# Kernel tuning notes

Measured on AMD Instinct MI355X. Metric: run time of the kernel, lower is better.

## Reference

```python
import jax, jax.numpy as jnp
import numpy as np
import math

F = 64        # num_features (multiplicity of each irrep)
N = 16000     # nodes
E = 256000    # edges (avg_num_neighbors = 16)
S = 4         # num_species
DE = 32       # scalar edge feature dim (radial basis)
W = 128       # interaction_mlp_width
AVG_NEIGH = 16.0
SQ2 = math.sqrt(2.0)
SQ3 = math.sqrt(3.0)


def setup_inputs() -> dict:
    key = jax.random.key(0)
    ks = jax.random.split(key, 32)
    def nrm(k, shape, scale=1.0):
        return jax.random.normal(k, shape, dtype=jnp.float32) * scale
    inp = {}
    # forward args
    inp["vectors"] = nrm(ks[0], (E, 1, 3))
    inp["lengths"] = jax.random.uniform(ks[1], (E, 1), dtype=jnp.float32)
    inp["node_s"] = nrm(ks[2], (N, F))            # 64x0e part of node_feats
    inp["node_v"] = nrm(ks[3], (N, F, 3))         # 64x1o part of node_feats
    inp["scalar_edge_feats"] = nrm(ks[4], (E, DE))
    inp["node_specie"] = jax.random.randint(ks[5], (N,), 0, S)
    inp["senders"] = jax.random.randint(ks[6], (E,), 0, N)
    inp["receivers"] = jax.random.randint(ks[7], (E,), 0, N)
    # parameters (e3nn Linear = per-irrep channel mixing, fan-in normalized; bias only on 0e)
    inp["W_up_s"] = nrm(ks[8], (F, F), F ** -0.5); inp["b_up_s"] = jnp.zeros((F,), jnp.float32)
    inp["W_up_v"] = nrm(ks[9], (F, F), F ** -0.5)
    din = 2 * F + DE + 1
    inp["mlp_W1"] = nrm(ks[10], (din, W), din ** -0.5); inp["mlp_b1"] = jnp.zeros((W,), jnp.float32)
    inp["mlp_W2"] = nrm(ks[11], (W, W), W ** -0.5); inp["mlp_b2"] = jnp.zeros((W,), jnp.float32)
    inp["mlp_W3"] = nrm(ks[12], (W, 3 * F), W ** -0.5); inp["mlp_b3"] = jnp.zeros((3 * F,), jnp.float32)
    inp["W_dn_s"] = nrm(ks[13], (F, F), F ** -0.5); inp["b_dn_s"] = jnp.zeros((F,), jnp.float32)
    inp["W_dn_v"] = nrm(ks[14], (2 * F, F), (2 * F) ** -0.5)
    # symmetric contraction weights (per species, per channel); correlation=2
    inp["w_sc_s"] = nrm(ks[15], (S, 3, F), 3 ** -0.5)   # paths to 0e: x0, x0^2, (x1.x1)/sqrt3
    inp["w_sc_v"] = nrm(ks[16], (S, 2, F), 2 ** -0.5)   # paths to 1o: x1, x0*x1
    inp["W_pb_s"] = nrm(ks[17], (F, F), F ** -0.5); inp["b_pb_s"] = jnp.zeros((F,), jnp.float32)
    inp["W_pb_v"] = nrm(ks[18], (F, F), F ** -0.5)
    inp["W_r1_s"] = nrm(ks[19], (F, 2 * F), F ** -0.5); inp["b_r1_s"] = jnp.zeros((2 * F,), jnp.float32)
    inp["W_r1_v"] = nrm(ks[20], (F, F), F ** -0.5)
    inp["W_r2_s"] = nrm(ks[21], (F, 1), F ** -0.5); inp["b_r2"] = jnp.zeros((1,), jnp.float32)
    inp["W_r2_v"] = nrm(ks[22], (F, 1), F ** -0.5)
    return inp


def reference(vectors, lengths, node_s, node_v, scalar_edge_feats, node_specie,
              senders, receivers,
              W_up_s, b_up_s, W_up_v,
              mlp_W1, mlp_b1, mlp_W2, mlp_b2, mlp_W3, mlp_b3,
              W_dn_s, b_dn_s, W_dn_v,
              w_sc_s, w_sc_v, W_pb_s, b_pb_s, W_pb_v,
              W_r1_s, b_r1_s, W_r1_v, W_r2_s, b_r2, W_r2_v):
    n = node_s.shape[0]
    # --- spherical harmonics, sh_irreps='1o', component normalization, normalize=False ---
    edge_v = SQ3 * vectors[:, 0, :]                              # [E,3]

    # --- InteractionBlock: linear_up ---
    h_s = node_s @ W_up_s + b_up_s                               # [N,F]
    h_v = jnp.einsum('nfi,fg->ngi', node_v, W_up_v)              # [N,F,3]

    # --- MessagePassingConvolution ---
    m_s = h_s[senders]                                           # [E,F] 0e
    m_v = h_v[senders]                                           # [E,F,3] 1o
    # tensor product with edge 1o, filtered to 0e+1o (unitary CG):
    tp_s = jnp.einsum('efi,ei->ef', m_v, edge_v) / SQ3           # 1o x 1o -> 0e  [E,F]
    tp_v1 = m_s[:, :, None] * edge_v[:, None, :]                 # 0e x 1o -> 1o  [E,F,3]
    tp_v2 = jnp.cross(m_v, edge_v[:, None, :]) / SQ2             # 1o x 1o -> 1o  [E,F,3]
    # scalar MLP mix (one scalar weight per output irrep = 3F)
    mlp_in = jnp.concatenate([m_s, h_s[receivers], scalar_edge_feats, lengths], axis=1)
    h = jax.nn.silu(mlp_in @ mlp_W1 + mlp_b1)
    h = jax.nn.silu(h @ mlp_W2 + mlp_b2)
    mix = h @ mlp_W3 + mlp_b3                                    # [E,3F]
    mix_s, mix_v1, mix_v2 = mix[:, :F], mix[:, F:2 * F], mix[:, 2 * F:]
    tp_s = tp_s * mix_s
    tp_v = jnp.concatenate([tp_v1 * mix_v1[:, :, None], tp_v2 * mix_v2[:, :, None]], axis=1)  # [E,2F,3]
    # scatter-add to receivers, normalize by avg_num_neighbors
    agg_s = jax.ops.segment_sum(tp_s, receivers, num_segments=n) / AVG_NEIGH   # [N,F]
    agg_v = jax.ops.segment_sum(tp_v, receivers, num_segments=n) / AVG_NEIGH   # [N,2F,3]
    # linear_down
    f_s = agg_s @ W_dn_s + b_dn_s                                # [N,F]
    f_v = jnp.einsum('nfi,fg->ngi', agg_v, W_dn_v)               # [N,F,3]

    # --- EquivariantProductBasisBlock: symmetric contraction (correlation=2), per-species ---
    ws = w_sc_s[node_specie]                                     # [N,3,F]
    wv = w_sc_v[node_specie]                                     # [N,2,F]
    vv = jnp.sum(f_v * f_v, axis=-1) / SQ3                       # 1o (x) 1o -> 0e, symmetric
    sc_s = ws[:, 0] * f_s + ws[:, 1] * (f_s * f_s) + ws[:, 2] * vv           # [N,F]
    sc_v = wv[:, 0][:, :, None] * f_v + wv[:, 1][:, :, None] * (f_s[:, :, None] * f_v)  # [N,F,3]
    p_s = sc_s @ W_pb_s + b_pb_s                                 # node_feats 0e out
    p_v = jnp.einsum('nfi,fg->ngi', sc_v, W_pb_v)                # node_feats 1o out

    # --- NonLinearReadoutBlock: linear to (2F x 0e + F x 1o), gate, linear to 1x0e+1x1o ---
    r_s = p_s @ W_r1_s + b_r1_s                                  # [N,2F]
    r_v = jnp.einsum('nfi,fg->ngi', p_v, W_r1_v)                 # [N,F,3]
    act = jax.nn.silu(r_s[:, :F])
    gates = jax.nn.silu(r_s[:, F:])
    g_v = gates[:, :, None] * r_v                                # gated vectors
    out_s = act @ W_r2_s + b_r2                                  # [N,1]  0e output
    out_v = jnp.einsum('nfi,fo->noi', g_v, W_r2_v)               # [N,1,3] 1o output
    return out_s, out_v, p_s, p_v
```

## Files before the change

kernel.cpp:

```cpp
#include <hip/hip_runtime.h>

typedef short bf16x8 __attribute__((ext_vector_type(8)));
typedef float f32x4  __attribute__((ext_vector_type(4)));
typedef unsigned short ushort_t;

__device__ __forceinline__ float silu(float x) {
    float t = __expf(-x);
    return x * __builtin_amdgcn_rcpf(1.f + t);
}

__device__ __forceinline__ ushort_t f2bs(float x) {
    union { float f; unsigned int u; } v; v.f = x;
    unsigned int r = v.u + 0x7FFF + ((v.u >> 16) & 1);
    return (ushort_t)(r >> 16);
}
__device__ __forceinline__ ushort_t f2bs_t(float x) {
    union { float f; unsigned int u; } v; v.f = x;
    return (ushort_t)(v.u >> 16);
}
__device__ __forceinline__ float bs2f(ushort_t x) {
    union { unsigned int u; float f; } v; v.u = ((unsigned int)x) << 16; return v.f;
}

constexpr int N_   = 16000;
constexpr int E_   = 256000;
constexpr int Fd   = 64;

constexpr float SQ3f    = 1.7320508075688772f;
constexpr float INV_SQ3 = 0.5773502691896258f;
constexpr float INV_SQ2 = 0.7071067811865476f;
constexpr float INV_AVG = 0.0625f;

constexpr int OFF_OS = 0;
constexpr int OFF_OV = N_;
constexpr int OFF_PS = OFF_OV + 3 * N_;
constexpr int OFF_PV = OFF_PS + N_ * Fd;

constexpr int W1P_SZ = 6 * 8 * 512;
constexpr int W2P_SZ = 4 * 8 * 512;
constexpr int W3P_SZ = 4 * 12 * 512;

__global__ __launch_bounds__(256) void pack_kernel(
    const float* __restrict__ W1, const float* __restrict__ W2,
    const float* __restrict__ W3,
    ushort_t* __restrict__ W1p, ushort_t* __restrict__ W2p,
    ushort_t* __restrict__ W3p)
{
    int idx = blockIdx.x * 256 + threadIdx.x;
    if (idx < W1P_SZ) {
        int j = idx & 7, lane = (idx >> 3) & 63, tile = idx >> 9;
        int c = tile >> 3, t = tile & 7;
        int k = c * 32 + (lane >> 4) * 8 + j;
        int n = t * 16 + (lane & 15);
        W1p[idx] = f2bs(k < 161 ? W1[k * 128 + n] : 0.f);
    } else if (idx < W1P_SZ + W2P_SZ) {
        int q = idx - W1P_SZ;
        int j = q & 7, lane = (q >> 3) & 63, tile = q >> 9;
        int c = tile >> 3, t = tile & 7;
        int k = c * 32 + (lane >> 4) * 8 + j;
        int n = t * 16 + (lane & 15);
        W2p[q] = f2bs(W2[k * 128 + n]);
    } else {
        int q = idx - W1P_SZ - W2P_SZ;
        int j = q & 7, lane = (q >> 3) & 63, tile = q >> 9;
        int c = tile / 12, t = tile % 12;
        int k = c * 32 + (lane >> 4) * 8 + j;
        int n = t * 16 + (lane & 15);
        W3p[q] = f2bs(W3[k * 192 + n]);
    }
}

__global__ __launch_bounds__(64) void up_kernel(
    const float* __restrict__ node_s, const float* __restrict__ node_v,
    const float* __restrict__ W_up_s, const float* __restrict__ b_up_s,
    const float* __restrict__ W_up_v,
    const int* __restrict__ receivers, int* __restrict__ cnt,
    ushort_t* __restrict__ hs_bf, float* __restrict__ h_v)
{
    __shared__ float ns[Fd];
    __shared__ float nv[Fd][3];
    const int n = blockIdx.x;
    const int g = threadIdx.x;

    if (g < 16) {
        int e = n * 16 + g;
        atomicAdd(&cnt[receivers[e]], 1);
    }

    ns[g] = node_s[n * Fd + g];
    for (int idx = g; idx < Fd * 3; idx += 64)
        nv[idx / 3][idx % 3] = node_v[n * Fd * 3 + idx];
    __syncthreads();

    float as = b_up_s[g];
    float a0 = 0.f, a1 = 0.f, a2 = 0.f;
    #pragma unroll 8
    for (int f = 0; f < Fd; f++) {
        float wss = W_up_s[f * Fd + g];
        as += ns[f] * wss;
        float wv = W_up_v[f * Fd + g];
        a0 += nv[f][0] * wv;
        a1 += nv[f][1] * wv;
        a2 += nv[f][2] * wv;
    }
    hs_bf[n * Fd + g] = f2bs(as);
    h_v[n * 192 + 0 * 64 + g] = a0;
    h_v[n * 192 + 1 * 64 + g] = a1;
    h_v[n * 192 + 2 * 64 + g] = a2;
}

__global__ __launch_bounds__(1024) void scan_kernel(
    const int* __restrict__ cnt, int* __restrict__ base, int* __restrict__ cursor)
{
    __shared__ int part[1024];
    const int t = threadIdx.x;
    int v[16];
    int s = 0;
    if (t < 1000) {
        const int4* c4 = (const int4*)(cnt + t * 16);
        #pragma unroll
        for (int q = 0; q < 4; q++) {
            int4 w = c4[q];
            v[q * 4 + 0] = w.x; v[q * 4 + 1] = w.y;
            v[q * 4 + 2] = w.z; v[q * 4 + 3] = w.w;
            s += w.x + w.y + w.z + w.w;
        }
    }
    part[t] = s;
    __syncthreads();
    for (int off = 1; off < 1024; off <<= 1) {
        int u = (t >= off) ? part[t - off] : 0;
        __syncthreads();
        part[t] += u;
        __syncthreads();
    }
    if (t < 1000) {
        int run = part[t] - s;
        int b[16];
        #pragma unroll
        for (int i = 0; i < 16; i++) { b[i] = run; run += v[i]; }
        int4* bb = (int4*)(base + t * 16);
        int4* cc = (int4*)(cursor + t * 16);
        #pragma unroll
        for (int q = 0; q < 4; q++) {
            int4 w = { b[q * 4], b[q * 4 + 1], b[q * 4 + 2], b[q * 4 + 3] };
            bb[q] = w;
            cc[q] = w;
        }
    }
}

__global__ __launch_bounds__(256, 6) void edge_mlp_kernel(
    const float* __restrict__ lengths, const float* __restrict__ sef,
    const int* __restrict__ senders, const int* __restrict__ receivers,
    const float* __restrict__ b1f, const float* __restrict__ b2f,
    const float* __restrict__ b3f,
    const ushort_t* __restrict__ hs_bf,
    const ushort_t* __restrict__ W1p, const ushort_t* __restrict__ W2p,
    const ushort_t* __restrict__ W3p,
    int* __restrict__ cursor, int* __restrict__ sorted_eid,
    ushort_t* __restrict__ tpx)
{
    __shared__ ushort_t Hs[64 * 136];

    const int tid  = threadIdx.x;
    const int wave = tid >> 6, lane = tid & 63;
    const int quad = lane >> 4, l4 = lane & 15;
    const int ebase = blockIdx.x * 64 + wave * 16;
    const int me    = ebase + l4;
    const int hrow  = wave * 16;

    if (tid < 64) {
        int e = blockIdx.x * 64 + tid;
        int p = atomicAdd(&cursor[receivers[e]], 1);
        sorted_eid[p] = e;
    }

    const int snd = senders[me];
    const int rcv = receivers[me];

    bf16x8 a[6];
    a[0] = *(const bf16x8*)(hs_bf + snd * 64 + quad * 8);
    a[1] = *(const bf16x8*)(hs_bf + snd * 64 + 32 + quad * 8);
    a[2] = *(const bf16x8*)(hs_bf + rcv * 64 + quad * 8);
    a[3] = *(const bf16x8*)(hs_bf + rcv * 64 + 32 + quad * 8);
    {
        const float4 s0 = *(const float4*)(sef + (size_t)me * 32 + quad * 8);
        const float4 s1 = *(const float4*)(sef + (size_t)me * 32 + quad * 8 + 4);
        bf16x8 t;
        t[0] = (short)f2bs(s0.x); t[1] = (short)f2bs(s0.y);
        t[2] = (short)f2bs(s0.z); t[3] = (short)f2bs(s0.w);
        t[4] = (short)f2bs(s1.x); t[5] = (short)f2bs(s1.y);
        t[6] = (short)f2bs(s1.z); t[7] = (short)f2bs(s1.w);
        a[4] = t;
    }
    {
        bf16x8 t = {0, 0, 0, 0, 0, 0, 0, 0};
        if (quad == 0) t[0] = (short)f2bs(lengths[me]);
        a[5] = t;
    }

    const bf16x8* B1 = (const bf16x8*)W1p;
    const bf16x8* B2 = (const bf16x8*)W2p;
    const bf16x8* B3 = (const bf16x8*)W3p;

    f32x4 acc[8];
    #pragma unroll
    for (int t = 0; t < 8; t++) acc[t] = (f32x4){0.f, 0.f, 0.f, 0.f};
    #pragma unroll
    for (int c = 0; c < 6; c++) {
        #pragma unroll
        for (int t = 0; t < 8; t++)
            acc[t] = __builtin_amdgcn_mfma_f32_16x16x32_bf16(
                a[c], B1[(c * 8 + t) * 64 + lane], acc[t], 0, 0, 0);
    }
    #pragma unroll
    for (int t = 0; t < 8; t++) {
        float bb = b1f[t * 16 + l4];
        #pragma unroll
        for (int r = 0; r < 4; r++)
            Hs[(hrow + quad * 4 + r) * 136 + t * 16 + l4] = f2bs_t(silu(acc[t][r] + bb));
    }

    #pragma unroll
    for (int t = 0; t < 8; t++) acc[t] = (f32x4){0.f, 0.f, 0.f, 0.f};
    #pragma unroll
    for (int c = 0; c < 4; c++) {
        bf16x8 af = *(const bf16x8*)(&Hs[(hrow + l4) * 136 + c * 32 + quad * 8]);
        #pragma unroll
        for (int t = 0; t < 8; t++)
            acc[t] = __builtin_amdgcn_mfma_f32_16x16x32_bf16(
                af, B2[(c * 8 + t) * 64 + lane], acc[t], 0, 0, 0);
    }
    #pragma unroll
    for (int t = 0; t < 8; t++) {
        float bb = b2f[t * 16 + l4];
        #pragma unroll
        for (int r = 0; r < 4; r++)
            Hs[(hrow + quad * 4 + r) * 136 + t * 16 + l4] = f2bs_t(silu(acc[t][r] + bb));
    }

    f32x4 acc3[12];
    #pragma unroll
    for (int t = 0; t < 12; t++) acc3[t] = (f32x4){0.f, 0.f, 0.f, 0.f};
    #pragma unroll
    for (int c = 0; c < 4; c++) {
        bf16x8 af = *(const bf16x8*)(&Hs[(hrow + l4) * 136 + c * 32 + quad * 8]);
        #pragma unroll
        for (int t = 0; t < 12; t++)
            acc3[t] = __builtin_amdgcn_mfma_f32_16x16x32_bf16(
                af, B3[(c * 12 + t) * 64 + lane], acc3[t], 0, 0, 0);
    }
    #pragma unroll
    for (int t = 0; t < 12; t++) {
        float bb = b3f[t * 16 + l4];
        #pragma unroll
        for (int r = 0; r < 4; r++)
            tpx[(size_t)(ebase + quad * 4 + r) * 192 + t * 16 + l4] =
                f2bs(acc3[t][r] + bb);
    }
}

__global__ __launch_bounds__(64, 8) void node_fused_kernel(
    const int* __restrict__ base, const int* __restrict__ cnt,
    const int* __restrict__ sorted_eid, const int* __restrict__ senders,
    const float* __restrict__ vectors,
    const ushort_t* __restrict__ tpx,
    const ushort_t* __restrict__ hs_bf, const float* __restrict__ h_v,
    const int* __restrict__ specie,
    const float* __restrict__ W_dn_s, const float* __restrict__ b_dn_s,
    const float* __restrict__ W_dn_v,
    const float* __restrict__ w_sc_s, const float* __restrict__ w_sc_v,
    const float* __restrict__ W_pb_s, const float* __restrict__ b_pb_s,
    const float* __restrict__ W_pb_v,
    const float* __restrict__ W_r1_s, const float* __restrict__ b_r1_s,
    const float* __restrict__ W_r1_v,
    const float* __restrict__ W_r2_s, const float* __restrict__ b_r2,
    const float* __restrict__ W_r2_v,
    float* __restrict__ out)
{
    __shared__ float as_l[Fd];
    __shared__ float av_l[2 * Fd][3];
    __shared__ float scs[Fd];
    __shared__ float scv[Fd][3];
    __shared__ float ps[Fd];
    __shared__ float pv[Fd][3];
    __shared__ int   eids[64];

    const int n = blockIdx.x;
    const int g = threadIdx.x;

    const int b = base[n];
    const int c = cnt[n];
    float accS = 0.f;
    float a10 = 0.f, a11 = 0.f, a12 = 0.f;
    float a20 = 0.f, a21 = 0.f, a22 = 0.f;

    for (int done = 0; done < c; done += 64) {
        int m = min(64, c - done);
        __syncthreads();
        if (g < m) eids[g] = sorted_eid[b + done + g];
        __syncthreads();
        for (int i = 0; i < m; i++) {
            const int e  = eids[i];
            const int se = senders[e];
            const float ev0 = SQ3f * vectors[e * 3 + 0];
            const float ev1 = SQ3f * vectors[e * 3 + 1];
            const float ev2 = SQ3f * vectors[e * 3 + 2];
            const float mv0 = h_v[(size_t)se * 192 + 0 * 64 + g];
            const float mv1 = h_v[(size_t)se * 192 + 1 * 64 + g];
            const float mv2 = h_v[(size_t)se * 192 + 2 * 64 + g];
            const float m_s = bs2f(hs_bf[se * 64 + g]);
            const ushort_t* mrow = tpx + (size_t)e * 192;
            const float c0 = bs2f(mrow[g]);
            const float c1 = bs2f(mrow[64 + g]);
            const float c2 = bs2f(mrow[128 + g]);

            float dot = mv0 * ev0 + mv1 * ev1 + mv2 * ev2;
            accS += dot * c0;
            float k1 = m_s * c1;
            a10 += k1 * ev0; a11 += k1 * ev1; a12 += k1 * ev2;
            a20 += (mv1 * ev2 - mv2 * ev1) * c2;
            a21 += (mv2 * ev0 - mv0 * ev2) * c2;
            a22 += (mv0 * ev1 - mv1 * ev0) * c2;
        }
    }
    as_l[g] = accS * (INV_SQ3 * INV_AVG);
    av_l[g][0] = a10 * INV_AVG;
    av_l[g][1] = a11 * INV_AVG;
    av_l[g][2] = a12 * INV_AVG;
    av_l[64 + g][0] = a20 * (INV_SQ2 * INV_AVG);
    av_l[64 + g][1] = a21 * (INV_SQ2 * INV_AVG);
    av_l[64 + g][2] = a22 * (INV_SQ2 * INV_AVG);
    __syncthreads();

    float f_s = b_dn_s[g];
    #pragma unroll 8
    for (int f = 0; f < Fd; f++) f_s += as_l[f] * W_dn_s[f * Fd + g];
    float fv0 = 0.f, fv1 = 0.f, fv2 = 0.f;
    #pragma unroll 8
    for (int f = 0; f < 2 * Fd; f++) {
        float w = W_dn_v[f * Fd + g];
        fv0 += av_l[f][0] * w;
        fv1 += av_l[f][1] * w;
        fv2 += av_l[f][2] * w;
    }

    float vv = (fv0 * fv0 + fv1 * fv1 + fv2 * fv2) * INV_SQ3;
    int sp = specie[n];
    float ws0 = w_sc_s[sp * 3 * Fd + 0 * Fd + g];
    float ws1 = w_sc_s[sp * 3 * Fd + 1 * Fd + g];
    float ws2 = w_sc_s[sp * 3 * Fd + 2 * Fd + g];
    float wv0 = w_sc_v[sp * 2 * Fd + 0 * Fd + g];
    float wv1 = w_sc_v[sp * 2 * Fd + 1 * Fd + g];
    float sc_s = ws0 * f_s + ws1 * f_s * f_s + ws2 * vv;
    float kv = wv0 + wv1 * f_s;
    scs[g] = sc_s;
    scv[g][0] = kv * fv0;
    scv[g][1] = kv * fv1;
    scv[g][2] = kv * fv2;
    __syncthreads();

    float p_s = b_pb_s[g];
    float pv0 = 0.f, pv1 = 0.f, pv2 = 0.f;
    #pragma unroll 8
    for (int f = 0; f < Fd; f++) {
        float wps = W_pb_s[f * Fd + g];
        p_s += scs[f] * wps;
        float wpv = W_pb_v[f * Fd + g];
        pv0 += scv[f][0] * wpv;
        pv1 += scv[f][1] * wpv;
        pv2 += scv[f][2] * wpv;
    }
    ps[g] = p_s;
    pv[g][0] = pv0; pv[g][1] = pv1; pv[g][2] = pv2;

    out[OFF_PS + n * Fd + g] = p_s;
    out[OFF_PV + (size_t)n * Fd * 3 + g * 3 + 0] = pv0;
    out[OFF_PV + (size_t)n * Fd * 3 + g * 3 + 1] = pv1;
    out[OFF_PV + (size_t)n * Fd * 3 + g * 3 + 2] = pv2;
    __syncthreads();

    float r0 = b_r1_s[g];
    float r1 = b_r1_s[g + Fd];
    float rv0 = 0.f, rv1 = 0.f, rv2 = 0.f;
    #pragma unroll 8
    for (int f = 0; f < Fd; f++) {
        float p = ps[f];
        r0 += p * W_r1_s[f * 2 * Fd + g];
        r1 += p * W_r1_s[f * 2 * Fd + g + Fd];
        float wrv = W_r1_v[f * Fd + g];
        rv0 += pv[f][0] * wrv;
        rv1 += pv[f][1] * wrv;
        rv2 += pv[f][2] * wrv;
    }
    float act  = silu(r0);
    float gate = silu(r1);
    float o_s = act * W_r2_s[g];
    float wr2v = W_r2_v[g];
    float ov0 = gate * rv0 * wr2v;
    float ov1 = gate * rv1 * wr2v;
    float ov2 = gate * rv2 * wr2v;

    #pragma unroll
    for (int off = 32; off > 0; off >>= 1) {
        o_s += __shfl_down(o_s, off);
        ov0 += __shfl_down(ov0, off);
        ov1 += __shfl_down(ov1, off);
        ov2 += __shfl_down(ov2, off);
    }
    if (g == 0) {
        out[OFF_OS + n] = o_s + b_r2[0];
        out[OFF_OV + n * 3 + 0] = ov0;
        out[OFF_OV + n * 3 + 1] = ov1;
        out[OFF_OV + n * 3 + 2] = ov2;
    }
}

extern "C" void kernel_launch(void* const* d_in, const int* in_sizes, int n_in,
                              void* d_out, int out_size, void* d_ws, size_t ws_size,
                              hipStream_t stream)
{
    const float* vectors  = (const float*)d_in[0];
    const float* lengths  = (const float*)d_in[1];
    const float* node_s   = (const float*)d_in[2];
    const float* node_v   = (const float*)d_in[3];
    const float* sef      = (const float*)d_in[4];
    const int*  specie    = (const int*)d_in[5];
    const int*  senders   = (const int*)d_in[6];
    const int*  receivers = (const int*)d_in[7];
    const float* W_up_s   = (const float*)d_in[8];
    const float* b_up_s   = (const float*)d_in[9];
    const float* W_up_v   = (const float*)d_in[10];
    const float* mlp_W1   = (const float*)d_in[11];
    const float* mlp_b1   = (const float*)d_in[12];
    const float* mlp_W2   = (const float*)d_in[13];
    const float* mlp_b2   = (const float*)d_in[14];
    const float* mlp_W3   = (const float*)d_in[15];
    const float* mlp_b3   = (const float*)d_in[16];
    const float* W_dn_s   = (const float*)d_in[17];
    const float* b_dn_s   = (const float*)d_in[18];
    const float* W_dn_v   = (const float*)d_in[19];
    const float* w_sc_s   = (const float*)d_in[20];
    const float* w_sc_v   = (const float*)d_in[21];
    const float* W_pb_s   = (const float*)d_in[22];
    const float* b_pb_s   = (const float*)d_in[23];
    const float* W_pb_v   = (const float*)d_in[24];
    const float* W_r1_s   = (const float*)d_in[25];
    const float* b_r1_s   = (const float*)d_in[26];
    const float* W_r1_v   = (const float*)d_in[27];
    const float* W_r2_s   = (const float*)d_in[28];
    const float* b_r2     = (const float*)d_in[29];
    const float* W_r2_v   = (const float*)d_in[30];

    float* h_v = (float*)d_ws;
    ushort_t* tpx   = (ushort_t*)(h_v + (size_t)N_ * 192);
    ushort_t* hs_bf = tpx + (size_t)E_ * 192;
    ushort_t* W1p   = hs_bf + (size_t)N_ * 64;
    ushort_t* W2p   = W1p + W1P_SZ;
    ushort_t* W3p   = W2p + W2P_SZ;
    int* cnt        = (int*)((((size_t)(W3p + W3P_SZ)) + 15) & ~(size_t)15);
    int* base       = cnt + N_;
    int* cursor     = base + N_;
    int* sorted_eid = cursor + N_;

    float* out = (float*)d_out;

    hipMemsetAsync(cnt, 0, N_ * sizeof(int), stream);

    up_kernel<<<N_, 64, 0, stream>>>(node_s, node_v, W_up_s, b_up_s, W_up_v,
                                     receivers, cnt, hs_bf, h_v);
    pack_kernel<<<256, 256, 0, stream>>>(mlp_W1, mlp_W2, mlp_W3, W1p, W2p, W3p);
    scan_kernel<<<1, 1024, 0, stream>>>(cnt, base, cursor);

    edge_mlp_kernel<<<E_ / 64, 256, 0, stream>>>(
        lengths, sef, senders, receivers,
        mlp_b1, mlp_b2, mlp_b3,
        hs_bf, W1p, W2p, W3p, cursor, sorted_eid, tpx);

    node_fused_kernel<<<N_, 64, 0, stream>>>(
        base, cnt, sorted_eid, senders, vectors,
        tpx, hs_bf, h_v, specie,
        W_dn_s, b_dn_s, W_dn_v, w_sc_s, w_sc_v,
        W_pb_s, b_pb_s, W_pb_v, W_r1_s, b_r1_s, W_r1_v,
        W_r2_s, b_r2, W_r2_v, out);
}
```

Measured before the change: 413.6 us.

## Process multiple nodes/edges per wave to reuse weight loads across rows

The up and node kernels now handle four nodes per 64-thread block, so each weight element loaded from global memory is reused across four nodes. The edge MLP gives each wave 32 edges (two 16-row MFMA tiles) sharing each B fragment, with 128-thread blocks. This cuts repeated weight traffic and block count in exchange for more registers, lower occupancy, and serialized per-node edge loops in the node kernel.

```diff
diff --git a/kernel.cpp b/kernel.cpp
--- a/kernel.cpp
+++ b/kernel.cpp
@@ -70,43 +70,54 @@
     }
 }
 
-__global__ __launch_bounds__(64) void up_kernel(
+__global__ __launch_bounds__(64, 4) void up_kernel(
     const float* __restrict__ node_s, const float* __restrict__ node_v,
     const float* __restrict__ W_up_s, const float* __restrict__ b_up_s,
     const float* __restrict__ W_up_v,
     const int* __restrict__ receivers, int* __restrict__ cnt,
     ushort_t* __restrict__ hs_bf, float* __restrict__ h_v)
 {
-    __shared__ float ns[Fd];
-    __shared__ float nv[Fd][3];
-    const int n = blockIdx.x;
-    const int g = threadIdx.x;
-
-    if (g < 16) {
-        int e = n * 16 + g;
+    __shared__ float ns[4][64];
+    __shared__ float nv[4][64][3];
+    const int n0 = blockIdx.x * 4;
+    const int g  = threadIdx.x;
+
+    {
+        int e = blockIdx.x * 64 + g;
         atomicAdd(&cnt[receivers[e]], 1);
     }
 
-    ns[g] = node_s[n * Fd + g];
-    for (int idx = g; idx < Fd * 3; idx += 64)
-        nv[idx / 3][idx % 3] = node_v[n * Fd * 3 + idx];
+    #pragma unroll
+    for (int j = 0; j < 4; j++) ns[j][g] = node_s[(n0 + j) * 64 + g];
+    for (int idx = g; idx < 4 * 192; idx += 64) {
+        int j = idx / 192, r = idx - j * 192;
+        nv[j][r / 3][r % 3] = node_v[(size_t)n0 * 192 + idx];
+    }
     __syncthreads();
 
-    float as = b_up_s[g];
-    float a0 = 0.f, a1 = 0.f, a2 = 0.f;
-    #pragma unroll 8
-    for (int f = 0; f < Fd; f++) {
-        float wss = W_up_s[f * Fd + g];
-        as += ns[f] * wss;
-        float wv = W_up_v[f * Fd + g];
-        a0 += nv[f][0] * wv;
-        a1 += nv[f][1] * wv;
-        a2 += nv[f][2] * wv;
-    }
-    hs_bf[n * Fd + g] = f2bs(as);
-    h_v[n * 192 + 0 * 64 + g] = a0;
-    h_v[n * 192 + 1 * 64 + g] = a1;
-    h_v[n * 192 + 2 * 64 + g] = a2;
+    float as[4], a0[4], a1[4], a2[4];
+    float bb = b_up_s[g];
+    #pragma unroll
+    for (int j = 0; j < 4; j++) { as[j] = bb; a0[j] = a1[j] = a2[j] = 0.f; }
+    #pragma unroll 4
+    for (int f = 0; f < 64; f++) {
+        float wss = W_up_s[f * 64 + g];
+        float wv  = W_up_v[f * 64 + g];
+        #pragma unroll
+        for (int j = 0; j < 4; j++) {
+            as[j] += ns[j][f] * wss;
+            a0[j] += nv[j][f][0] * wv;
+            a1[j] += nv[j][f][1] * wv;
+            a2[j] += nv[j][f][2] * wv;
+        }
+    }
+    #pragma unroll
+    for (int j = 0; j < 4; j++) {
+        hs_bf[(n0 + j) * 64 + g] = f2bs(as[j]);
+        h_v[(n0 + j) * 192 + 0 * 64 + g] = a0[j];
+        h_v[(n0 + j) * 192 + 1 * 64 + g] = a1[j];
+        h_v[(n0 + j) * 192 + 2 * 64 + g] = a2[j];
+    }
 }
 
 __global__ __launch_bounds__(1024) void scan_kernel(
@@ -150,7 +161,7 @@
     }
 }
 
-__global__ __launch_bounds__(256, 6) void edge_mlp_kernel(
+__global__ __launch_bounds__(128, 2) void edge_mlp_kernel(
     const float* __restrict__ lengths, const float* __restrict__ sef,
     const int* __restrict__ senders, const int* __restrict__ receivers,
     const float* __restrict__ b1f, const float* __restrict__ b2f,
@@ -166,9 +177,10 @@
     const int tid  = threadIdx.x;
     const int wave = tid >> 6, lane = tid & 63;
     const int quad = lane >> 4, l4 = lane & 15;
-    const int ebase = blockIdx.x * 64 + wave * 16;
-    const int me    = ebase + l4;
-    const int hrow  = wave * 16;
+    const int ebase = blockIdx.x * 64 + wave * 32;
+    const int me0   = ebase + l4;
+    const int me1   = ebase + 16 + l4;
+    const int hrow  = wave * 32;
 
     if (tid < 64) {
         int e = blockIdx.x * 64 + tid;
@@ -176,92 +188,117 @@
         sorted_eid[p] = e;
     }
 
-    const int snd = senders[me];
-    const int rcv = receivers[me];
-
-    bf16x8 a[6];
-    a[0] = *(const bf16x8*)(hs_bf + snd * 64 + quad * 8);
-    a[1] = *(const bf16x8*)(hs_bf + snd * 64 + 32 + quad * 8);
-    a[2] = *(const bf16x8*)(hs_bf + rcv * 64 + quad * 8);
-    a[3] = *(const bf16x8*)(hs_bf + rcv * 64 + 32 + quad * 8);
+    const int snd0 = senders[me0], rcv0 = receivers[me0];
+    const int snd1 = senders[me1], rcv1 = receivers[me1];
+
+    bf16x8 a0[6], a1[6];
+    a0[0] = *(const bf16x8*)(hs_bf + snd0 * 64 + quad * 8);
+    a0[1] = *(const bf16x8*)(hs_bf + snd0 * 64 + 32 + quad * 8);
+    a0[2] = *(const bf16x8*)(hs_bf + rcv0 * 64 + quad * 8);
+    a0[3] = *(const bf16x8*)(hs_bf + rcv0 * 64 + 32 + quad * 8);
+    a1[0] = *(const bf16x8*)(hs_bf + snd1 * 64 + quad * 8);
+    a1[1] = *(const bf16x8*)(hs_bf + snd1 * 64 + 32 + quad * 8);
+    a1[2] = *(const bf16x8*)(hs_bf + rcv1 * 64 + quad * 8);
+    a1[3] = *(const bf16x8*)(hs_bf + rcv1 * 64 + 32 + quad * 8);
     {
-        const float4 s0 = *(const float4*)(sef + (size_t)me * 32 + quad * 8);
-        const float4 s1 = *(const float4*)(sef + (size_t)me * 32 + quad * 8 + 4);
+        const float4 s0 = *(const float4*)(sef + (size_t)me0 * 32 + quad * 8);
+        const float4 s1 = *(const float4*)(sef + (size_t)me0 * 32 + quad * 8 + 4);
         bf16x8 t;
         t[0] = (short)f2bs(s0.x); t[1] = (short)f2bs(s0.y);
         t[2] = (short)f2bs(s0.z); t[3] = (short)f2bs(s0.w);
         t[4] = (short)f2bs(s1.x); t[5] = (short)f2bs(s1.y);
         t[6] = (short)f2bs(s1.z); t[7] = (short)f2bs(s1.w);
-        a[4] = t;
+        a0[4] = t;
+        const float4 u0 = *(const float4*)(sef + (size_t)me1 * 32 + quad * 8);
+        const float4 u1 = *(const float4*)(sef + (size_t)me1 * 32 + quad * 8 + 4);
+        t[0] = (short)f2bs(u0.x); t[1] = (short)f2bs(u0.y);
+        t[2] = (short)f2bs(u0.z); t[3] = (short)f2bs(u0.w);
+        t[4] = (short)f2bs(u1.x); t[5] = (short)f2bs(u1.y);
+        t[6] = (short)f2bs(u1.z); t[7] = (short)f2bs(u1.w);
+        a1[4] = t;
     }
     {
-        bf16x8 t = {0, 0, 0, 0, 0, 0, 0, 0};
-        if (quad == 0) t[0] = (short)f2bs(lengths[me]);
-        a[5] = t;
+        bf16x8 t = {0,0,0,0,0,0,0,0};
+        bf16x8 u = {0,0,0,0,0,0,0,0};
+        if (quad == 0) { t[0] = (short)f2bs(lengths[me0]); u[0] = (short)f2bs(lengths[me1]); }
+        a0[5] = t; a1[5] = u;
     }
 
     const bf16x8* B1 = (const bf16x8*)W1p;
     const bf16x8* B2 = (const bf16x8*)W2p;
     const bf16x8* B3 = (const bf16x8*)W3p;
 
-    f32x4 acc[8];
-    #pragma unroll
-    for (int t = 0; t < 8; t++) acc[t] = (f32x4){0.f, 0.f, 0.f, 0.f};
+    f32x4 accA[8], accB[8];
+    #pragma unroll
+    for (int t = 0; t < 8; t++) { accA[t] = (f32x4){0,0,0,0}; accB[t] = (f32x4){0,0,0,0}; }
     #pragma unroll
     for (int c = 0; c < 6; c++) {
         #pragma unroll
-        for (int t = 0; t < 8; t++)
-            acc[t] = __builtin_amdgcn_mfma_f32_16x16x32_bf16(
-                a[c], B1[(c * 8 + t) * 64 + lane], acc[t], 0, 0, 0);
+        for (int t = 0; t < 8; t++) {
+            bf16x8 b = B1[(c * 8 + t) * 64 + lane];
+            accA[t] = __builtin_amdgcn_mfma_f32_16x16x32_bf16(a0[c], b, accA[t], 0, 0, 0);
+            accB[t] = __builtin_amdgcn_mfma_f32_16x16x32_bf16(a1[c], b, accB[t], 0, 0, 0);
+        }
     }
     #pragma unroll
     for (int t = 0; t < 8; t++) {
         float bb = b1f[t * 16 + l4];
         #pragma unroll
-        for (int r = 0; r < 4; r++)
-            Hs[(hrow + quad * 4 + r) * 136 + t * 16 + l4] = f2bs_t(silu(acc[t][r] + bb));
-    }
-
-    #pragma unroll
-    for (int t = 0; t < 8; t++) acc[t] = (f32x4){0.f, 0.f, 0.f, 0.f};
+        for (int r = 0; r < 4; r++) {
+            Hs[(hrow + quad * 4 + r) * 136 + t * 16 + l4]      = f2bs_t(silu(accA[t][r] + bb));
+            Hs[(hrow + 16 + quad * 4 + r) * 136 + t * 16 + l4] = f2bs_t(silu(accB[t][r] + bb));
+        }
+    }
+
+    #pragma unroll
+    for (int t = 0; t < 8; t++) { accA[t] = (f32x4){0,0,0,0}; accB[t] = (f32x4){0,0,0,0}; }
     #pragma unroll
     for (int c = 0; c < 4; c++) {
-        bf16x8 af = *(const bf16x8*)(&Hs[(hrow + l4) * 136 + c * 32 + quad * 8]);
-        #pragma unroll
-        for (int t = 0; t < 8; t++)
-            acc[t] = __builtin_amdgcn_mfma_f32_16x16x32_bf16(
-                af, B2[(c * 8 + t) * 64 + lane], acc[t], 0, 0, 0);
+        bf16x8 af0 = *(const bf16x8*)(&Hs[(hrow + l4) * 136 + c * 32 + quad * 8]);
+        bf16x8 af1 = *(const bf16x8*)(&Hs[(hrow + 16 + l4) * 136 + c * 32 + quad * 8]);
+        #pragma unroll
+        for (int t = 0; t < 8; t++) {
+            bf16x8 b = B2[(c * 8 + t) * 64 + lane];
+            accA[t] = __builtin_amdgcn_mfma_f32_16x16x32_bf16(af0, b, accA[t], 0, 0, 0);
+            accB[t] = __builtin_amdgcn_mfma_f32_16x16x32_bf16(af1, b, accB[t], 0, 0, 0);
+        }
     }
     #pragma unroll
     for (int t = 0; t < 8; t++) {
         float bb = b2f[t * 16 + l4];
         #pragma unroll
-        for (int r = 0; r < 4; r++)
-            Hs[(hrow + quad * 4 + r) * 136 + t * 16 + l4] = f2bs_t(silu(acc[t][r] + bb));
-    }
-
-    f32x4 acc3[12];
-    #pragma unroll
-    for (int t = 0; t < 12; t++) acc3[t] = (f32x4){0.f, 0.f, 0.f, 0.f};
+        for (int r = 0; r < 4; r++) {
+            Hs[(hrow + quad * 4 + r) * 136 + t * 16 + l4]      = f2bs_t(silu(accA[t][r] + bb));
+            Hs[(hrow + 16 + quad * 4 + r) * 136 + t * 16 + l4] = f2bs_t(silu(accB[t][r] + bb));
+        }
+    }
+
+    f32x4 acc3A[12], acc3B[12];
+    #pragma unroll
+    for (int t = 0; t < 12; t++) { acc3A[t] = (f32x4){0,0,0,0}; acc3B[t] = (f32x4){0,0,0,0}; }
     #pragma unroll
     for (int c = 0; c < 4; c++) {
-        bf16x8 af = *(const bf16x8*)(&Hs[(hrow + l4) * 136 + c * 32 + quad * 8]);
-        #pragma unroll
-        for (int t = 0; t < 12; t++)
-            acc3[t] = __builtin_amdgcn_mfma_f32_16x16x32_bf16(
-                af, B3[(c * 12 + t) * 64 + lane], acc3[t], 0, 0, 0);
+        bf16x8 af0 = *(const bf16x8*)(&Hs[(hrow + l4) * 136 + c * 32 + quad * 8]);
+        bf16x8 af1 = *(const bf16x8*)(&Hs[(hrow + 16 + l4) * 136 + c * 32 + quad * 8]);
+        #pragma unroll
+        for (int t = 0; t < 12; t++) {
+            bf16x8 b = B3[(c * 12 + t) * 64 + lane];
+            acc3A[t] = __builtin_amdgcn_mfma_f32_16x16x32_bf16(af0, b, acc3A[t], 0, 0, 0);
+            acc3B[t] = __builtin_amdgcn_mfma_f32_16x16x32_bf16(af1, b, acc3B[t], 0, 0, 0);
+        }
     }
     #pragma unroll
     for (int t = 0; t < 12; t++) {
         float bb = b3f[t * 16 + l4];
         #pragma unroll
-        for (int r = 0; r < 4; r++)
-            tpx[(size_t)(ebase + quad * 4 + r) * 192 + t * 16 + l4] =
-                f2bs(acc3[t][r] + bb);
-    }
-}
-
-__global__ __launch_bounds__(64, 8) void node_fused_kernel(
+        for (int r = 0; r < 4; r++) {
+            tpx[(size_t)(ebase + quad * 4 + r) * 192 + t * 16 + l4]      = f2bs(acc3A[t][r] + bb);
+            tpx[(size_t)(ebase + 16 + quad * 4 + r) * 192 + t * 16 + l4] = f2bs(acc3B[t][r] + bb);
+        }
+    }
+}
+
+__global__ __launch_bounds__(64, 4) void node_fused_kernel(
     const int* __restrict__ base, const int* __restrict__ cnt,
     const int* __restrict__ sorted_eid, const int* __restrict__ senders,
     const float* __restrict__ vectors,
@@ -279,141 +316,177 @@
     const float* __restrict__ W_r2_v,
     float* __restrict__ out)
 {
-    __shared__ float as_l[Fd];
-    __shared__ float av_l[2 * Fd][3];
-    __shared__ float scs[Fd];
-    __shared__ float scv[Fd][3];
-    __shared__ float ps[Fd];
-    __shared__ float pv[Fd][3];
+    __shared__ float as_l[4][64];
+    __shared__ float av_l[4][128][3];
+    __shared__ float scs[4][64];
+    __shared__ float scv[4][64][3];
+    __shared__ float ps_[4][64];
+    __shared__ float pv_[4][64][3];
     __shared__ int   eids[64];
 
-    const int n = blockIdx.x;
-    const int g = threadIdx.x;
-
-    const int b = base[n];
-    const int c = cnt[n];
-    float accS = 0.f;
-    float a10 = 0.f, a11 = 0.f, a12 = 0.f;
-    float a20 = 0.f, a21 = 0.f, a22 = 0.f;
-
-    for (int done = 0; done < c; done += 64) {
-        int m = min(64, c - done);
-        __syncthreads();
-        if (g < m) eids[g] = sorted_eid[b + done + g];
-        __syncthreads();
-        for (int i = 0; i < m; i++) {
-            const int e  = eids[i];
-            const int se = senders[e];
-            const float ev0 = SQ3f * vectors[e * 3 + 0];
-            const float ev1 = SQ3f * vectors[e * 3 + 1];
-            const float ev2 = SQ3f * vectors[e * 3 + 2];
-            const float mv0 = h_v[(size_t)se * 192 + 0 * 64 + g];
-            const float mv1 = h_v[(size_t)se * 192 + 1 * 64 + g];
-            const float mv2 = h_v[(size_t)se * 192 + 2 * 64 + g];
-            const float m_s = bs2f(hs_bf[se * 64 + g]);
-            const ushort_t* mrow = tpx + (size_t)e * 192;
-            const float c0 = bs2f(mrow[g]);
-            const float c1 = bs2f(mrow[64 + g]);
-            const float c2 = bs2f(mrow[128 + g]);
-
-            float dot = mv0 * ev0 + mv1 * ev1 + mv2 * ev2;
-            accS += dot * c0;
-            float k1 = m_s * c1;
-            a10 += k1 * ev0; a11 += k1 * ev1; a12 += k1 * ev2;
-            a20 += (mv1 * ev2 - mv2 * ev1) * c2;
-            a21 += (mv2 * ev0 - mv0 * ev2) * c2;
-            a22 += (mv0 * ev1 - mv1 * ev0) * c2;
-        }
-    }
-    as_l[g] = accS * (INV_SQ3 * INV_AVG);
-    av_l[g][0] = a10 * INV_AVG;
-    av_l[g][1] = a11 * INV_AVG;
-    av_l[g][2] = a12 * INV_AVG;
-    av_l[64 + g][0] = a20 * (INV_SQ2 * INV_AVG);
-    av_l[64 + g][1] = a21 * (INV_SQ2 * INV_AVG);
-    av_l[64 + g][2] = a22 * (INV_SQ2 * INV_AVG);
+    const int n0 = blockIdx.x * 4;
+    const int g  = threadIdx.x;
+
+    for (int j = 0; j < 4; j++) {
+        const int n = n0 + j;
+        const int b = base[n];
+        const int c = cnt[n];
+        float accS = 0.f;
+        float a10 = 0.f, a11 = 0.f, a12 = 0.f;
+        float a20 = 0.f, a21 = 0.f, a22 = 0.f;
+
+        for (int done = 0; done < c; done += 64) {
+            int m = min(64, c - done);
+            __syncthreads();
+            if (g < m) eids[g] = sorted_eid[b + done + g];
+            __syncthreads();
+            for (int i = 0; i < m; i++) {
+                const int e  = eids[i];
+                const int se = senders[e];
+                const float ev0 = SQ3f * vectors[e * 3 + 0];
+                const float ev1 = SQ3f * vectors[e * 3 + 1];
+                const float ev2 = SQ3f * vectors[e * 3 + 2];
+                const float mv0 = h_v[(size_t)se * 192 + 0 * 64 + g];
+                const float mv1 = h_v[(size_t)se * 192 + 1 * 64 + g];
+                const float mv2 = h_v[(size_t)se * 192 + 2 * 64 + g];
+                const float m_s = bs2f(hs_bf[se * 64 + g]);
+                const ushort_t* mrow = tpx + (size_t)e * 192;
+                const float c0 = bs2f(mrow[g]);
+                const float c1 = bs2f(mrow[64 + g]);
+                const float c2 = bs2f(mrow[128 + g]);
+
+                float dot = mv0 * ev0 + mv1 * ev1 + mv2 * ev2;
+                accS += dot * c0;
+                float k1 = m_s * c1;
+                a10 += k1 * ev0; a11 += k1 * ev1; a12 += k1 * ev2;
+                a20 += (mv1 * ev2 - mv2 * ev1) * c2;
+                a21 += (mv2 * ev0 - mv0 * ev2) * c2;
+                a22 += (mv0 * ev1 - mv1 * ev0) * c2;
+            }
+        }
+        as_l[j][g] = accS * (INV_SQ3 * INV_AVG);
+        av_l[j][g][0] = a10 * INV_AVG;
+        av_l[j][g][1] = a11 * INV_AVG;
+        av_l[j][g][2] = a12 * INV_AVG;
+        av_l[j][64 + g][0] = a20 * (INV_SQ2 * INV_AVG);
+        av_l[j][64 + g][1] = a21 * (INV_SQ2 * INV_AVG);
+        av_l[j][64 + g][2] = a22 * (INV_SQ2 * INV_AVG);
+    }
     __syncthreads();
 
-    float f_s = b_dn_s[g];
-    #pragma unroll 8
-    for (int f = 0; f < Fd; f++) f_s += as_l[f] * W_dn_s[f * Fd + g];
-    float fv0 = 0.f, fv1 = 0.f, fv2 = 0.f;
-    #pragma unroll 8
-    for (int f = 0; f < 2 * Fd; f++) {
-        float w = W_dn_v[f * Fd + g];
-        fv0 += av_l[f][0] * w;
-        fv1 += av_l[f][1] * w;
-        fv2 += av_l[f][2] * w;
-    }
-
-    float vv = (fv0 * fv0 + fv1 * fv1 + fv2 * fv2) * INV_SQ3;
-    int sp = specie[n];
-    float ws0 = w_sc_s[sp * 3 * Fd + 0 * Fd + g];
-    float ws1 = w_sc_s[sp * 3 * Fd + 1 * Fd + g];
-    float ws2 = w_sc_s[sp * 3 * Fd + 2 * Fd + g];
-    float wv0 = w_sc_v[sp * 2 * Fd + 0 * Fd + g];
-    float wv1 = w_sc_v[sp * 2 * Fd + 1 * Fd + g];
-    float sc_s = ws0 * f_s + ws1 * f_s * f_s + ws2 * vv;
-    float kv = wv0 + wv1 * f_s;
-    scs[g] = sc_s;
-    scv[g][0] = kv * fv0;
-    scv[g][1] = kv * fv1;
-    scv[g][2] = kv * fv2;
+    float f_s[4];
+    {
+        float bb = b_dn_s[g];
+        #pragma unroll
+        for (int j = 0; j < 4; j++) f_s[j] = bb;
+    }
+    #pragma unroll 4
+    for (int f = 0; f < 64; f++) {
+        float w = W_dn_s[f * 64 + g];
+        #pragma unroll
+        for (int j = 0; j < 4; j++) f_s[j] += as_l[j][f] * w;
+    }
+    float fv[4][3] = {};
+    #pragma unroll 4
+    for (int f = 0; f < 128; f++) {
+        float w = W_dn_v[f * 64 + g];
+        #pragma unroll
+        for (int j = 0; j < 4; j++) {
+            fv[j][0] += av_l[j][f][0] * w;
+            fv[j][1] += av_l[j][f][1] * w;
+            fv[j][2] += av_l[j][f][2] * w;
+        }
+    }
+
+    #pragma unroll
+    for (int j = 0; j < 4; j++) {
+        float vv = (fv[j][0]*fv[j][0] + fv[j][1]*fv[j][1] + fv[j][2]*fv[j][2]) * INV_SQ3;
+        int sp = specie[n0 + j];
+        float ws0 = w_sc_s[sp * 192 + 0 * 64 + g];
+        float ws1 = w_sc_s[sp * 192 + 1 * 64 + g];
+        float ws2 = w_sc_s[sp * 192 + 2 * 64 + g];
+        float wv0 = w_sc_v[sp * 128 + 0 * 64 + g];
+        float wv1 = w_sc_v[sp * 128 + 1 * 64 + g];
+        float sc = ws0 * f_s[j] + ws1 * f_s[j] * f_s[j] + ws2 * vv;
+        float kv = wv0 + wv1 * f_s[j];
+        scs[j][g] = sc;
+        scv[j][g][0] = kv * fv[j][0];
+        scv[j][g][1] = kv * fv[j][1];
+        scv[j][g][2] = kv * fv[j][2];
+    }
     __syncthreads();
 
-    float p_s = b_pb_s[g];
-    float pv0 = 0.f, pv1 = 0.f, pv2 = 0.f;
-    #pragma unroll 8
-    for (int f = 0; f < Fd; f++) {
-        float wps = W_pb_s[f * Fd + g];
-        p_s += scs[f] * wps;
-        float wpv = W_pb_v[f * Fd + g];
-        pv0 += scv[f][0] * wpv;
-        pv1 += scv[f][1] * wpv;
-        pv2 += scv[f][2] * wpv;
-    }
-    ps[g] = p_s;
-    pv[g][0] = pv0; pv[g][1] = pv1; pv[g][2] = pv2;
-
-    out[OFF_PS + n * Fd + g] = p_s;
-    out[OFF_PV + (size_t)n * Fd * 3 + g * 3 + 0] = pv0;
-    out[OFF_PV + (size_t)n * Fd * 3 + g * 3 + 1] = pv1;
-    out[OFF_PV + (size_t)n * Fd * 3 + g * 3 + 2] = pv2;
+    float p_s[4], pv[4][3] = {};
+    {
+        float bb = b_pb_s[g];
+        #pragma unroll
+        for (int j = 0; j < 4; j++) p_s[j] = bb;
+    }
+    #pragma unroll 4
+    for (int f = 0; f < 64; f++) {
+        float wps = W_pb_s[f * 64 + g];
+        float wpv = W_pb_v[f * 64 + g];
+        #pragma unroll
+        for (int j = 0; j < 4; j++) {
+            p_s[j] += scs[j][f] * wps;
+            pv[j][0] += scv[j][f][0] * wpv;
+            pv[j][1] += scv[j][f][1] * wpv;
+            pv[j][2] += scv[j][f][2] * wpv;
+        }
+    }
+    #pragma unroll
+    for (int j = 0; j < 4; j++) {
+        ps_[j][g] = p_s[j];
+        pv_[j][g][0] = pv[j][0]; pv_[j][g][1] = pv[j][1]; pv_[j][g][2] = pv[j][2];
+        out[OFF_PS + (n0 + j) * 64 + g] = p_s[j];
+        out[OFF_PV + (size_t)(n0 + j) * 192 + g * 3 + 0] = pv[j][0];
+        out[OFF_PV + (size_t)(n0 + j) * 192 + g * 3 + 1] = pv[j][1];
+        out[OFF_PV + (size_t)(n0 + j) * 192 + g * 3 + 2] = pv[j][2];
+    }
     __syncthreads();
 
-    float r0 = b_r1_s[g];
-    float r1 = b_r1_s[g + Fd];
-    float rv0 = 0.f, rv1 = 0.f, rv2 = 0.f;
-    #pragma unroll 8
-    for (int f = 0; f < Fd; f++) {
-        float p = ps[f];
-        r0 += p * W_r1_s[f * 2 * Fd + g];
-        r1 += p * W_r1_s[f * 2 * Fd + g + Fd];
-        float wrv = W_r1_v[f * Fd + g];
-        rv0 += pv[f][0] * wrv;
-        rv1 += pv[f][1] * wrv;
-        rv2 += pv[f][2] * wrv;
-    }
-    float act  = silu(r0);
-    float gate = silu(r1);
-    float o_s = act * W_r2_s[g];
-    float wr2v = W_r2_v[g];
-    float ov0 = gate * rv0 * wr2v;
-    float ov1 = gate * rv1 * wr2v;
-    float ov2 = gate * rv2 * wr2v;
-
-    #pragma unroll
-    for (int off = 32; off > 0; off >>= 1) {
-        o_s += __shfl_down(o_s, off);
-        ov0 += __shfl_down(ov0, off);
-        ov1 += __shfl_down(ov1, off);
-        ov2 += __shfl_down(ov2, off);
-    }
-    if (g == 0) {
-        out[OFF_OS + n] = o_s + b_r2[0];
-        out[OFF_OV + n * 3 + 0] = ov0;
-        out[OFF_OV + n * 3 + 1] = ov1;
-        out[OFF_OV + n * 3 + 2] = ov2;
+    float r0[4], r1[4], rv[4][3] = {};
+    {
+        float bb0 = b_r1_s[g], bb1 = b_r1_s[g + 64];
+        #pragma unroll
+        for (int j = 0; j < 4; j++) { r0[j] = bb0; r1[j] = bb1; }
+    }
+    #pragma unroll 4
+    for (int f = 0; f < 64; f++) {
+        float w0 = W_r1_s[f * 128 + g];
+        float w1 = W_r1_s[f * 128 + g + 64];
+        float wv = W_r1_v[f * 64 + g];
+        #pragma unroll
+        for (int j = 0; j < 4; j++) {
+            float p = ps_[j][f];
+            r0[j] += p * w0;
+            r1[j] += p * w1;
+            rv[j][0] += pv_[j][f][0] * wv;
+            rv[j][1] += pv_[j][f][1] * wv;
+            rv[j][2] += pv_[j][f][2] * wv;
+        }
+    }
+    float wr2s = W_r2_s[g], wr2v = W_r2_v[g];
+    #pragma unroll
+    for (int j = 0; j < 4; j++) {
+        float o_s = silu(r0[j]) * wr2s;
+        float gate = silu(r1[j]);
+        float ov0 = gate * rv[j][0] * wr2v;
+        float ov1 = gate * rv[j][1] * wr2v;
+        float ov2 = gate * rv[j][2] * wr2v;
+        #pragma unroll
+        for (int off = 32; off > 0; off >>= 1) {
+            o_s += __shfl_down(o_s, off);
+            ov0 += __shfl_down(ov0, off);
+            ov1 += __shfl_down(ov1, off);
+            ov2 += __shfl_down(ov2, off);
+        }
+        if (g == 0) {
+            out[OFF_OS + n0 + j] = o_s + b_r2[0];
+            out[OFF_OV + (n0 + j) * 3 + 0] = ov0;
+            out[OFF_OV + (n0 + j) * 3 + 1] = ov1;
+            out[OFF_OV + (n0 + j) * 3 + 2] = ov2;
+        }
     }
 }
 
@@ -468,17 +541,17 @@
 
     hipMemsetAsync(cnt, 0, N_ * sizeof(int), stream);
 
-    up_kernel<<<N_, 64, 0, stream>>>(node_s, node_v, W_up_s, b_up_s, W_up_v,
-                                     receivers, cnt, hs_bf, h_v);
+    up_kernel<<<N_ / 4, 64, 0, stream>>>(node_s, node_v, W_up_s, b_up_s, W_up_v,
+                                         receivers, cnt, hs_bf, h_v);
     pack_kernel<<<256, 256, 0, stream>>>(mlp_W1, mlp_W2, mlp_W3, W1p, W2p, W3p);
     scan_kernel<<<1, 1024, 0, stream>>>(cnt, base, cursor);
 
-    edge_mlp_kernel<<<E_ / 64, 256, 0, stream>>>(
+    edge_mlp_kernel<<<E_ / 64, 128, 0, stream>>>(
         lengths, sef, senders, receivers,
         mlp_b1, mlp_b2, mlp_b3,
         hs_bf, W1p, W2p, W3p, cursor, sorted_eid, tpx);
 
-    node_fused_kernel<<<N_, 64, 0, stream>>>(
+    node_fused_kernel<<<N_ / 4, 64, 0, stream>>>(
         base, cnt, sorted_eid, senders, vectors,
         tpx, hs_bf, h_v, specie,
         W_dn_s, b_dn_s, W_dn_v, w_sc_s, w_sc_v,
```

Result: slower. 490.0 us (+18.5%).
